# Kernel optimization log

Measured on AMD Instinct MI355X. Metric: run time of the kernel, lower is better.

The kernel has to match this reference:

```python
import jax, jax.numpy as jnp
import numpy as np

B, X, C = 8192, 8, 512        # batch, map_num, img_dim==tex_dim
P, Y = 8, 1000                # n_prompts, cls_num
FAKE = 16                     # fake prompt width (hardcoded in module)
F = 2048                      # feat_dim
CLS = 1000                    # cls_num
IN_DIM = P * X * FAKE         # 1024
SF = 64.0


def setup_inputs() -> dict:
    key = jax.random.key(0)
    ks = jax.random.split(key, 8)
    s = 0.02
    return {
        "img_f": jax.random.normal(ks[0], (B, X, C), jnp.float32),
        "tex_f": jax.random.normal(ks[1], (P, Y, C), jnp.float32),
        "fake_cls": jax.random.normal(ks[2], (P, FAKE, C), jnp.float32),
        "fc_w": jax.random.normal(ks[3], (C, C), jnp.float32) * s,
        "fc_b": jnp.zeros((C,), jnp.float32),
        "bn1_g": jnp.ones((IN_DIM,), jnp.float32),
        "bn1_b": jnp.zeros((IN_DIM,), jnp.float32),
        "w1": jax.random.normal(ks[4], (F, IN_DIM), jnp.float32) * s,
        "b1": jnp.zeros((F,), jnp.float32),
        "bn2_g": jnp.ones((F,), jnp.float32),
        "bn2_b": jnp.zeros((F,), jnp.float32),
        "w2": jax.random.normal(ks[5], (CLS, F), jnp.float32) * s,
        "b2": jnp.zeros((CLS,), jnp.float32),
    }


def _bn(x, g, b, eps=1e-5):
    # BatchNorm1d in training mode: batch mean / biased batch var
    m = x.mean(axis=0)
    v = x.var(axis=0)
    return (x - m) * jax.lax.rsqrt(v + eps) * g + b


def reference(img_f, tex_f, fake_cls, fc_w, fc_b, bn1_g, bn1_b, w1, b1,
              bn2_g, bn2_b, w2, b2):
    # independent L2 norm over feature dim, scaled by x_sf=64
    img_n = img_f / (jnp.linalg.norm(img_f, axis=-1, keepdims=True) + 1e-6) * SF
    tex_n = tex_f / (jnp.linalg.norm(tex_f, axis=-1, keepdims=True) + 1e-6) * SF
    # prompt attention over the class axis
    tex_fc = jnp.einsum('pyc,dc->pyd', tex_n, fc_w) + fc_b          # fc(tex_f)
    attn = jax.nn.softmax(jnp.einsum('pxc,pyc->pxy', fake_cls, tex_fc), axis=-1)
    tex_a = jnp.einsum('pxy,pyc->pxc', attn, tex_n)                  # (P,16,C)
    # cross-modal relation: 'b x c, y d c -> b yxd' (icomp/tcomp are Identity)
    cp = jnp.einsum('bxc,pdc->bpxd', img_n, tex_a).reshape(img_n.shape[0], -1)
    # prt_fc: BN -> Linear -> ELU -> BN -> Linear
    h = jax.nn.elu(_bn(cp, bn1_g, bn1_b) @ w1.T + b1)
    return _bn(h, bn2_g, bn2_b) @ w2.T + b2
```

## Files before the change

kernel.cpp:

```cpp
#include <hip/hip_runtime.h>
#include <math.h>


typedef __attribute__((ext_vector_type(8))) short bf16x8;
typedef __attribute__((ext_vector_type(4))) float f32x4;

__device__ __forceinline__ float waveSum(float v) {
#pragma unroll
    for (int o = 32; o > 0; o >>= 1) v += __shfl_xor(v, o);
    return v;
}
__device__ __forceinline__ float waveMax(float v) {
#pragma unroll
    for (int o = 32; o > 0; o >>= 1) v = fmaxf(v, __shfl_xor(v, o));
    return v;
}
__device__ __forceinline__ unsigned short f2bf(float x) {
    union { float f; unsigned u; } v; v.f = x;
    unsigned r = v.u + 0x7FFFu + ((v.u >> 16) & 1u);
    return (unsigned short)(r >> 16);
}
__device__ __forceinline__ float bf2f(unsigned short h) {
    union { unsigned u; float f; } v; v.u = ((unsigned)h) << 16; return v.f;
}
__device__ __forceinline__ void gload16(const void* g, const void* l) {
    __builtin_amdgcn_global_load_lds((const __attribute__((address_space(1))) void*)g,
                                     (__attribute__((address_space(3))) void*)l, 16, 0, 0);
}
__device__ __forceinline__ int xcd_swz(int d, int n) {
    int q = n >> 3;
    return (d & 7) * q + (d >> 3);
}
#define SBAR __builtin_amdgcn_sched_barrier(0)

__global__ __launch_bounds__(256) void k_prep(const float* __restrict__ tex_f,
                                              unsigned short* __restrict__ texn,
                                              const float* __restrict__ fake_cls,
                                              const float* __restrict__ fc_w,
                                              unsigned short* __restrict__ g_bf) {
    __shared__ float sred[4];
    __shared__ float fcls[512];
    int bid = blockIdx.x, t = threadIdx.x;
    if (bid < 8000) {
        const float* r = tex_f + (size_t)bid * 512;
        float2 v = *(const float2*)(r + t * 2);
        float ss = v.x * v.x + v.y * v.y;
        ss = waveSum(ss);
        if ((t & 63) == 0) sred[t >> 6] = ss;
        __syncthreads();
        float tot = sred[0] + sred[1] + sred[2] + sred[3];
        float sc = 64.f / (sqrtf(tot) + 1e-6f);
        unsigned u = (unsigned)f2bf(v.x * sc) | ((unsigned)f2bf(v.y * sc) << 16);
        *(unsigned*)(texn + (size_t)bid * 512 + t * 2) = u;
    } else {
        int row = bid - 8000;
        fcls[t]       = fake_cls[row * 512 + t];
        fcls[t + 256] = fake_cls[row * 512 + t + 256];
        __syncthreads();
        float a0 = 0.f, a1 = 0.f;
        for (int d = 0; d < 512; ++d) {
            float fv = fcls[d];
            a0 = fmaf(fv, fc_w[d * 512 + t], a0);
            a1 = fmaf(fv, fc_w[d * 512 + t + 256], a1);
        }
        g_bf[row * 512 + t]       = f2bf(a0);
        g_bf[row * 512 + t + 256] = f2bf(a1);
    }
}

__global__ __launch_bounds__(256) void k_wsum_sm(const float* __restrict__ logit,
                                                 const unsigned short* __restrict__ texn,
                                                 float* __restrict__ part) {
    int yt = blockIdx.x, p = blockIdx.y, t = threadIdx.x;
    int lane = t & 63, w = t >> 6;
    __shared__ float wl[16][63];
    __shared__ float ms[16], iss[16];
    const int y0 = yt * 63;
    const int ylen = min(63, 1000 - y0);
#pragma unroll
    for (int rr = 0; rr < 4; ++rr) {
        int x = w * 4 + rr;
        const float* lr = logit + ((size_t)p * 16 + x) * 1000;
        float m = -3.0e38f;
        for (int y = lane; y < 1000; y += 64) m = fmaxf(m, lr[y]);
        m = waveMax(m);
        float s = 0.f;
        for (int y = lane; y < 1000; y += 64) s += expf(lr[y] - m);
        s = waveSum(s);
        if (lane == 0) { ms[x] = m; iss[x] = 1.f / s; }
    }
    __syncthreads();
    for (int idx = t; idx < 16 * ylen; idx += 256) {
        int x = idx / ylen, y = idx % ylen;
        wl[x][y] = expf(logit[((size_t)p * 16 + x) * 1000 + y0 + y] - ms[x]) * iss[x];
    }
    __syncthreads();
    int c0 = t * 2;
    const unsigned short* tp = texn + ((size_t)p * 1000 + y0) * 512 + c0;
    float a0[16], a1[16];
#pragma unroll
    for (int x = 0; x < 16; ++x) { a0[x] = 0.f; a1[x] = 0.f; }
    for (int y = 0; y < ylen; ++y) {
        unsigned u = *(const unsigned*)(tp + (size_t)y * 512);
        float lo = bf2f((unsigned short)(u & 0xffff));
        float hi = bf2f((unsigned short)(u >> 16));
#pragma unroll
        for (int x = 0; x < 16; ++x) {
            float ww = wl[x][y];
            a0[x] = fmaf(ww, lo, a0[x]);
            a1[x] = fmaf(ww, hi, a1[x]);
        }
    }
#pragma unroll
    for (int x = 0; x < 16; ++x) {
        float* dst = part + ((size_t)((yt * 8 + p) * 16 + x)) * 512 + c0;
        dst[0] = a0[x];
        dst[1] = a1[x];
    }
}

__global__ __launch_bounds__(256) void k_texa_red(const float* __restrict__ part,
                                                  unsigned short* __restrict__ texa) {
    int row = blockIdx.x, t = threadIdx.x;
    int p = row >> 4, x = row & 15;
    int c = t * 2;
    float s0 = 0.f, s1 = 0.f;
#pragma unroll
    for (int yt = 0; yt < 16; ++yt) {
        const float* src = part + ((size_t)((yt * 8 + p) * 16 + x)) * 512 + c;
        s0 += src[0];
        s1 += src[1];
    }
    unsigned u = (unsigned)f2bf(s0) | ((unsigned)f2bf(s1) << 16);
    *(unsigned*)(texa + (size_t)row * 512 + c) = u;
}

__global__ __launch_bounds__(256) void k_colstat_bf(const unsigned short* __restrict__ src,
                                                    float* __restrict__ ps,
                                                    float* __restrict__ pq, int ncols) {
    int col = blockIdx.x * 256 + threadIdx.x;
    int r0 = blockIdx.y * 128;
    const unsigned short* p = src + (size_t)r0 * ncols + col;
    float s = 0.f, q = 0.f;
    for (int r = 0; r < 128; ++r) {
        float v = bf2f(p[(size_t)r * ncols]);
        s += v;
        q = fmaf(v, v, q);
    }
    ps[(size_t)blockIdx.y * ncols + col] = s;
    pq[(size_t)blockIdx.y * ncols + col] = q;
}

template <bool PERM>
__global__ __launch_bounds__(256) void k_bnfin(const float* __restrict__ ps,
                                               const float* __restrict__ pq,
                                               const float* __restrict__ gam,
                                               const float* __restrict__ bet,
                                               float* __restrict__ a, float* __restrict__ c,
                                               int ncols) {
    int col = blockIdx.x * 256 + threadIdx.x;
    float S = 0.f, Q = 0.f;
    for (int i = 0; i < 64; ++i) {
        S += ps[(size_t)i * ncols + col];
        Q += pq[(size_t)i * ncols + col];
    }
    float mean = S * (1.f / 8192.f);
    float var = Q * (1.f / 8192.f) - mean * mean;
    int j = col;
    if (PERM) {
        int x = col >> 7, jj = col & 127, pp = jj >> 4, d = jj & 15;
        j = (pp << 7) + (x << 4) + d;
    }
    float av = gam[j] * rsqrtf(var + 1e-5f);
    a[col] = av;
    c[col] = bet[j] - mean * av;
}

template <bool PERM>
__global__ __launch_bounds__(256) void k_foldw_bf(const float* __restrict__ W,
                                                  const float* __restrict__ bin,
                                                  const float* __restrict__ a,
                                                  const float* __restrict__ c,
                                                  unsigned short* __restrict__ Wout,
                                                  float* __restrict__ bout,
                                                  int Kdim, int nvalid) {
    int f = blockIdx.x, t = threadIdx.x;
    unsigned short* wo = Wout + (size_t)f * Kdim;
    if (f >= nvalid) {
        for (int col = t; col < Kdim; col += 256) wo[col] = 0;
        if (t == 0) bout[f] = 0.f;
        return;
    }
    const float* wr = W + (size_t)f * Kdim;
    float partial = 0.f;
    for (int col = t; col < Kdim; col += 256) {
        int j = col;
        if (PERM) {
            int x = col >> 7, jj = col & 127, pp = jj >> 4, d = jj & 15;
            j = (pp << 7) + (x << 4) + d;
        }
        float wv = wr[j];
        wo[col] = f2bf(wv * a[col]);
        partial = fmaf(wv, c[col], partial);
    }
    partial = waveSum(partial);
    __shared__ float sred[4];
    if ((t & 63) == 0) sred[t >> 6] = partial;
    __syncthreads();
    if (t == 0) bout[f] = bin[f] + sred[0] + sred[1] + sred[2] + sred[3];
}

template <int EPI, bool A_F32>
__global__ __launch_bounds__(256) void gemm_mfma(const void* __restrict__ Av,
                                                 const unsigned short* __restrict__ Bv,
                                                 void* __restrict__ Cv, int K,
                                                 int ntn, int ldc, int nvalid,
                                                 int aZ, int bZ, int cZ) {
    __shared__ unsigned short Asl[128 * 64];
    __shared__ unsigned short Bsl[128 * 64];
    __shared__ float rowinv[128];
    const int tid = threadIdx.x;
    const int lane = tid & 63, wid = tid >> 6;
    const int wr = wid >> 1, wc = wid & 1;
    const int wg = xcd_swz(blockIdx.x, gridDim.x);
    const int m0 = (wg / ntn) * 128, n0 = (wg % ntn) * 128;
    const int z = blockIdx.y;

    const float* Af = (const float*)Av;
    const unsigned short* Ab = (const unsigned short*)Av + (size_t)z * aZ;
    const unsigned short* B = Bv + (size_t)z * bZ;

    f32x4 acc[4][4];
#pragma unroll
    for (int i = 0; i < 4; ++i)
#pragma unroll
        for (int j = 0; j < 4; ++j) acc[i][j] = {0.f, 0.f, 0.f, 0.f};

    const int swz = ((lane & 7) ^ (lane >> 3)) * 8;
    const int lrow = lane & 15, lkh = lane >> 4;
    float ssq[4] = {0.f, 0.f, 0.f, 0.f};

    for (int k0 = 0; k0 < K; k0 += 64) {
        if (A_F32) {
#pragma unroll
            for (int r = 0; r < 4; ++r) {
                int row = r * 32 + (tid >> 3);
                int kk = (tid & 7) * 8;
                const float* src = Af + (size_t)(m0 + row) * K + k0 + kk;
                float4 p0 = *(const float4*)src;
                float4 p1 = *(const float4*)(src + 4);
                ssq[r] += p0.x*p0.x + p0.y*p0.y + p0.z*p0.z + p0.w*p0.w
                        + p1.x*p1.x + p1.y*p1.y + p1.z*p1.z + p1.w*p1.w;
                bf16x8 v;
                v[0] = (short)f2bf(p0.x); v[1] = (short)f2bf(p0.y);
                v[2] = (short)f2bf(p0.z); v[3] = (short)f2bf(p0.w);
                v[4] = (short)f2bf(p1.x); v[5] = (short)f2bf(p1.y);
                v[6] = (short)f2bf(p1.z); v[7] = (short)f2bf(p1.w);
                *(bf16x8*)&Asl[row * 64 + (kk ^ ((row & 7) << 3))] = v;
            }
        } else {
#pragma unroll
            for (int r = 0; r < 4; ++r) {
                int row = r * 32 + wid * 8 + (lane >> 3);
                gload16(Ab + (size_t)(m0 + row) * K + k0 + swz,
                        Asl + r * 2048 + wid * 512);
            }
        }
#pragma unroll
        for (int r = 0; r < 4; ++r) {
            int row = r * 32 + wid * 8 + (lane >> 3);
            gload16(B + (size_t)(n0 + row) * K + k0 + swz,
                    Bsl + r * 2048 + wid * 512);
        }
        __syncthreads();
#pragma unroll
        for (int kk = 0; kk < 2; ++kk) {
            bf16x8 af[4], bfr[4];
#pragma unroll
            for (int m = 0; m < 4; ++m) {
                int row = wr * 64 + m * 16 + lrow;
                af[m] = *(const bf16x8*)&Asl[row * 64 + ((kk * 32 + lkh * 8) ^ ((row & 7) << 3))];
            }
#pragma unroll
            for (int n = 0; n < 4; ++n) {
                int row = wc * 64 + n * 16 + lrow;
                bfr[n] = *(const bf16x8*)&Bsl[row * 64 + ((kk * 32 + lkh * 8) ^ ((row & 7) << 3))];
            }
#pragma unroll
            for (int m = 0; m < 4; ++m)
#pragma unroll
                for (int n = 0; n < 4; ++n)
                    acc[m][n] = __builtin_amdgcn_mfma_f32_16x16x32_bf16(af[m], bfr[n], acc[m][n], 0, 0, 0);
        }
        __syncthreads();
    }

    if (A_F32) {
#pragma unroll
        for (int r = 0; r < 4; ++r) {
            float s = ssq[r];
            s += __shfl_xor(s, 1); s += __shfl_xor(s, 2); s += __shfl_xor(s, 4);
            if ((tid & 7) == 0) rowinv[r * 32 + (tid >> 3)] = 64.f / (sqrtf(s) + 1e-6f);
        }
        __syncthreads();
    }

    const int colbase = n0 + wc * 64 + lrow;
    if (EPI == 0) {
        unsigned short* C = (unsigned short*)Cv;
#pragma unroll
        for (int m = 0; m < 4; ++m) {
            int rloc = wr * 64 + m * 16 + lkh * 4;
#pragma unroll
            for (int r = 0; r < 4; ++r) {
                float riv = rowinv[rloc + r];
#pragma unroll
                for (int n = 0; n < 4; ++n)
                    C[(size_t)(m0 + rloc + r) * ldc + colbase + n * 16] = f2bf(acc[m][n][r] * riv);
            }
        }
    } else {
        float* C = (float*)Cv + (size_t)z * cZ;
#pragma unroll
        for (int m = 0; m < 4; ++m) {
            int row = m0 + wr * 64 + m * 16 + lkh * 4;
#pragma unroll
            for (int r = 0; r < 4; ++r) {
                if ((row + r) >= 16) continue;
#pragma unroll
                for (int n = 0; n < 4; ++n) {
                    int col = colbase + n * 16;
                    if (col < nvalid) C[(size_t)(row + r) * ldc + col] = acc[m][n][r];
                }
            }
        }
    }
}

template <int FM, int NH, int EPI>
__global__ __launch_bounds__(512, 2) void gemm256(const unsigned short* __restrict__ A,
                                                  const unsigned short* __restrict__ B,
                                                  void* __restrict__ Cv, int K,
                                                  int ntn, int ldc, int nvalid,
                                                  const float* __restrict__ bias,
                                                  float* __restrict__ ps,
                                                  float* __restrict__ pq) {
    constexpr int BM = FM * 32;
    constexpr int MH = BM / 128;
    constexpr int BN = NH * 128;
    constexpr int LA = 2 * (MH + NH);
    __shared__ unsigned short Asl[2][MH][128 * 64];
    __shared__ unsigned short Bsl[2][NH][128 * 64];
    const int tid = threadIdx.x;
    const int lane = tid & 63, wid = tid >> 6;
    const int wm = wid >> 2, wn = wid & 3;
    const int wg = xcd_swz(blockIdx.x, gridDim.x);
    const int m0 = (wg / ntn) * BM, n0 = (wg % ntn) * BN;
    const int lrow = lane & 15, lkh = lane >> 4;
    const int l7 = lane & 7;
    const int ksrc = ((lane & 7) ^ (lane >> 3)) * 8;
    const int mbase = wm * (BM / 2);
    const int mhalf = mbase >> 7;
    const int mloc0 = mbase & 127;
    const int nbase = wn * 64;
    const int nhalf = nbase >> 7;
    const int nloc0 = nbase & 127;

    f32x4 acc[FM][4];
#pragma unroll
    for (int m = 0; m < FM; ++m)
#pragma unroll
        for (int n = 0; n < 4; ++n) acc[m][n] = {0.f, 0.f, 0.f, 0.f};

    const int nkt = K >> 6;

    auto stage = [&](int kt, int buf) {
#pragma unroll
        for (int hf = 0; hf < MH; ++hf)
#pragma unroll
            for (int j = 0; j < 2; ++j) {
                int rl = wid * 16 + j * 8 + (lane >> 3);
                gload16(A + (size_t)(m0 + hf * 128 + rl) * K + kt * 64 + ksrc,
                        &Asl[buf][hf][(wid * 16 + j * 8) * 64]);
            }
#pragma unroll
        for (int hf = 0; hf < NH; ++hf)
#pragma unroll
            for (int j = 0; j < 2; ++j) {
                int rl = wid * 16 + j * 8 + (lane >> 3);
                gload16(B + (size_t)(n0 + hf * 128 + rl) * K + kt * 64 + ksrc,
                        &Bsl[buf][hf][(wid * 16 + j * 8) * 64]);
            }
    };

    stage(0, 0);
    stage(1, 1);
    if constexpr (LA == 8) asm volatile("s_waitcnt vmcnt(8)" ::: "memory");
    else asm volatile("s_waitcnt vmcnt(6)" ::: "memory");
    SBAR; __builtin_amdgcn_s_barrier(); SBAR;

    for (int kt = 0; kt < nkt; ++kt) {
        const int cur = kt & 1;
        bf16x8 af0[FM], bf0[4];
#pragma unroll
        for (int m = 0; m < FM; ++m) {
            int row = mloc0 + m * 16 + lrow;
            af0[m] = *(const bf16x8*)&Asl[cur][mhalf][row * 64 + ((lkh ^ l7) << 3)];
        }
#pragma unroll
        for (int n = 0; n < 4; ++n) {
            int row = nloc0 + n * 16 + lrow;
            bf0[n] = *(const bf16x8*)&Bsl[cur][nhalf][row * 64 + ((lkh ^ l7) << 3)];
        }
        __builtin_amdgcn_s_setprio(1);
#pragma unroll
        for (int m = 0; m < FM; ++m)
#pragma unroll
            for (int n = 0; n < 4; ++n)
                acc[m][n] = __builtin_amdgcn_mfma_f32_16x16x32_bf16(af0[m], bf0[n], acc[m][n], 0, 0, 0);
        __builtin_amdgcn_s_setprio(0);
        bf16x8 af1[FM], bf1[4];
#pragma unroll
        for (int m = 0; m < FM; ++m) {
            int row = mloc0 + m * 16 + lrow;
            af1[m] = *(const bf16x8*)&Asl[cur][mhalf][row * 64 + (((4 + lkh) ^ l7) << 3)];
        }
#pragma unroll
        for (int n = 0; n < 4; ++n) {
            int row = nloc0 + n * 16 + lrow;
            bf1[n] = *(const bf16x8*)&Bsl[cur][nhalf][row * 64 + (((4 + lkh) ^ l7) << 3)];
        }
        if (kt + 1 < nkt) {
            asm volatile("s_waitcnt lgkmcnt(0)" ::: "memory");
            SBAR; __builtin_amdgcn_s_barrier(); SBAR;
            if (kt + 2 < nkt) {
                stage(kt + 2, cur);
                if constexpr (LA == 8) asm volatile("s_waitcnt vmcnt(8)" ::: "memory");
                else asm volatile("s_waitcnt vmcnt(6)" ::: "memory");
            } else {
                asm volatile("s_waitcnt vmcnt(0)" ::: "memory");
            }
            SBAR; __builtin_amdgcn_s_barrier(); SBAR;
        }
        __builtin_amdgcn_s_setprio(1);
#pragma unroll
        for (int m = 0; m < FM; ++m)
#pragma unroll
            for (int n = 0; n < 4; ++n)
                acc[m][n] = __builtin_amdgcn_mfma_f32_16x16x32_bf16(af1[m], bf1[n], acc[m][n], 0, 0, 0);
        __builtin_amdgcn_s_setprio(0);
    }

    const int colbase = n0 + nbase + lrow;
    if (EPI == 1) {
        unsigned short* C = (unsigned short*)Cv;
        float bv[4], sN[4] = {0.f, 0.f, 0.f, 0.f}, qN[4] = {0.f, 0.f, 0.f, 0.f};
#pragma unroll
        for (int n = 0; n < 4; ++n) bv[n] = bias[colbase + n * 16];
#pragma unroll
        for (int m = 0; m < FM; ++m) {
            int row = m0 + mbase + m * 16 + lkh * 4;
#pragma unroll
            for (int r = 0; r < 4; ++r)
#pragma unroll
                for (int n = 0; n < 4; ++n) {
                    float v = acc[m][n][r] + bv[n];
                    v = v > 0.f ? v : expm1f(v);
                    sN[n] += v;
                    qN[n] = fmaf(v, v, qN[n]);
                    C[(size_t)(row + r) * ldc + colbase + n * 16] = f2bf(v);
                }
        }
#pragma unroll
        for (int n = 0; n < 4; ++n) {
            sN[n] += __shfl_xor(sN[n], 16); sN[n] += __shfl_xor(sN[n], 32);
            qN[n] += __shfl_xor(qN[n], 16); qN[n] += __shfl_xor(qN[n], 32);
        }
        if (lane < 16) {
            int mt = wg / ntn;
#pragma unroll
            for (int n = 0; n < 4; ++n) {
                ps[(size_t)(mt * 2 + wm) * ldc + colbase + n * 16] = sN[n];
                pq[(size_t)(mt * 2 + wm) * ldc + colbase + n * 16] = qN[n];
            }
        }
    } else {
        float* C = (float*)Cv;
        float bv[4];
#pragma unroll
        for (int n = 0; n < 4; ++n) bv[n] = bias[colbase + n * 16];
#pragma unroll
        for (int m = 0; m < FM; ++m) {
            int row = m0 + mbase + m * 16 + lkh * 4;
#pragma unroll
            for (int r = 0; r < 4; ++r)
#pragma unroll
                for (int n = 0; n < 4; ++n) {
                    int col = colbase + n * 16;
                    if (col < nvalid) C[(size_t)(row + r) * ldc + col] = acc[m][n][r] + bv[n];
                }
        }
    }
}

extern "C" void kernel_launch(void* const* d_in, const int* in_sizes, int n_in,
                              void* d_out, int out_size, void* d_ws, size_t ws_size,
                              hipStream_t stream) {
    const float* img_f    = (const float*)d_in[0];
    const float* tex_f    = (const float*)d_in[1];
    const float* fake_cls = (const float*)d_in[2];
    const float* fc_w     = (const float*)d_in[3];
    const float* bn1_g    = (const float*)d_in[5];
    const float* bn1_b    = (const float*)d_in[6];
    const float* w1       = (const float*)d_in[7];
    const float* b1       = (const float*)d_in[8];
    const float* bn2_g    = (const float*)d_in[9];
    const float* bn2_b    = (const float*)d_in[10];
    const float* w2       = (const float*)d_in[11];
    const float* b2       = (const float*)d_in[12];
    float* out = (float*)d_out;

    char* w = (char*)d_ws;
    unsigned short* texn = (unsigned short*)(w);
    unsigned short* g_bf = (unsigned short*)(w + 8388608);
    float*          logit= (float*)(w + 8650752);
    float*          part = (float*)(w + 9175040);
    unsigned short* texa = (unsigned short*)(w + 13369344);
    unsigned short* cp   = (unsigned short*)(w + 13500416);
    unsigned short* w1a  = (unsigned short*)(w + 30277632);
    float*          b1p  = (float*)(w + 34471936);
    float*          a1   = (float*)(w + 34480128);
    float*          c1   = (float*)(w + 34484224);
    float*          ps   = (float*)(w + 34488320);
    float*          pq   = (float*)(w + 35012608);
    unsigned short* h    = (unsigned short*)(w + 35536896);
    unsigned short* w2a  = (unsigned short*)(w + 69091328);
    float*          b2p  = (float*)(w + 73285632);
    float*          a2   = (float*)(w + 73289728);
    float*          c2   = (float*)(w + 73297920);

    k_prep<<<8128, 256, 0, stream>>>(tex_f, texn, fake_cls, fc_w, g_bf);
    gemm_mfma<3, false><<<dim3(8, 8), 256, 0, stream>>>(
        g_bf, texn, logit, 512, 8, 1000, 1000, 16 * 512, 1000 * 512, 16 * 1000);
    k_wsum_sm<<<dim3(16, 8), 256, 0, stream>>>(logit, texn, part);
    k_texa_red<<<128, 256, 0, stream>>>(part, texa);

    gemm_mfma<0, true><<<dim3(512, 1), 256, 0, stream>>>(
        img_f, texa, cp, 512, 1, 128, 128, 0, 0, 0);

    k_colstat_bf<<<dim3(4, 64), 256, 0, stream>>>(cp, ps, pq, 1024);
    k_bnfin<true><<<4, 256, 0, stream>>>(ps, pq, bn1_g, bn1_b, a1, c1, 1024);
    k_foldw_bf<true><<<2048, 256, 0, stream>>>(w1, b1, a1, c1, w1a, b1p, 1024, 2048);

    gemm256<8, 2, 1><<<dim3(256), 512, 0, stream>>>(
        cp, w1a, h, 1024, 8, 2048, 2048, b1p, ps, pq);

    k_bnfin<false><<<8, 256, 0, stream>>>(ps, pq, bn2_g, bn2_b, a2, c2, 2048);
    k_foldw_bf<false><<<1024, 256, 0, stream>>>(w2, b2, a2, c2, w2a, b2p, 2048, 1000);

    gemm256<4, 2, 2><<<dim3(256), 512, 0, stream>>>(
        h, w2a, out, 2048, 4, 1000, 1000, b2p, nullptr, nullptr);
}
```

Before: 240.8 us.

## Interleave next-tile global loads with second-half MFMAs in gemm256 loop

Splits the tile staging into separate A and B load lambdas and issues them between two halves of the second-k-slice MFMA block, before the vmcnt wait and barrier. Previously all loads were issued and waited on before any of those MFMAs ran. The goal is to hide global-to-LDS load issue latency behind matrix math and shorten the sync bubble. It also hardcodes BN as 256, which assumes NH==2 for every instantiation, and it moves the MFMAs after the first barrier, which changes where the waves stall.

```diff
diff --git a/kernel.cpp b/kernel.cpp
--- a/kernel.cpp
+++ b/kernel.cpp
@@ -347,7 +347,6 @@
                                                   float* __restrict__ pq) {
     constexpr int BM = FM * 32;
     constexpr int MH = BM / 128;
-    constexpr int BN = NH * 128;
     constexpr int LA = 2 * (MH + NH);
     __shared__ unsigned short Asl[2][MH][128 * 64];
     __shared__ unsigned short Bsl[2][NH][128 * 64];
@@ -355,7 +354,7 @@
     const int lane = tid & 63, wid = tid >> 6;
     const int wm = wid >> 2, wn = wid & 3;
     const int wg = xcd_swz(blockIdx.x, gridDim.x);
-    const int m0 = (wg / ntn) * BM, n0 = (wg % ntn) * BN;
+    const int m0 = (wg / ntn) * BM, n0 = (wg % ntn) * 256;
     const int lrow = lane & 15, lkh = lane >> 4;
     const int l7 = lane & 7;
     const int ksrc = ((lane & 7) ^ (lane >> 3)) * 8;
@@ -374,7 +373,7 @@
 
     const int nkt = K >> 6;
 
-    auto stage = [&](int kt, int buf) {
+    auto stageA = [&](int kt, int buf) {
 #pragma unroll
         for (int hf = 0; hf < MH; ++hf)
 #pragma unroll
@@ -383,6 +382,8 @@
                 gload16(A + (size_t)(m0 + hf * 128 + rl) * K + kt * 64 + ksrc,
                         &Asl[buf][hf][(wid * 16 + j * 8) * 64]);
             }
+    };
+    auto stageB = [&](int kt, int buf) {
 #pragma unroll
         for (int hf = 0; hf < NH; ++hf)
 #pragma unroll
@@ -393,10 +394,9 @@
             }
     };
 
-    stage(0, 0);
-    stage(1, 1);
-    if constexpr (LA == 8) asm volatile("s_waitcnt vmcnt(8)" ::: "memory");
-    else asm volatile("s_waitcnt vmcnt(6)" ::: "memory");
+    stageA(0, 0); stageB(0, 0);
+    stageA(1, 1); stageB(1, 1);
+    asm volatile("s_waitcnt vmcnt(%0)" :: "i"(LA) : "memory");
     SBAR; __builtin_amdgcn_s_barrier(); SBAR;
 
     for (int kt = 0; kt < nkt; ++kt) {
@@ -433,22 +433,37 @@
         if (kt + 1 < nkt) {
             asm volatile("s_waitcnt lgkmcnt(0)" ::: "memory");
             SBAR; __builtin_amdgcn_s_barrier(); SBAR;
-            if (kt + 2 < nkt) {
-                stage(kt + 2, cur);
-                if constexpr (LA == 8) asm volatile("s_waitcnt vmcnt(8)" ::: "memory");
-                else asm volatile("s_waitcnt vmcnt(6)" ::: "memory");
-            } else {
-                asm volatile("s_waitcnt vmcnt(0)" ::: "memory");
-            }
+            const bool pf = (kt + 2 < nkt);
+            if (pf) stageA(kt + 2, cur);
+            SBAR;
+            __builtin_amdgcn_s_setprio(1);
+#pragma unroll
+            for (int m = 0; m < FM / 2; ++m)
+#pragma unroll
+                for (int n = 0; n < 4; ++n)
+                    acc[m][n] = __builtin_amdgcn_mfma_f32_16x16x32_bf16(af1[m], bf1[n], acc[m][n], 0, 0, 0);
+            __builtin_amdgcn_s_setprio(0);
+            if (pf) stageB(kt + 2, cur);
+            SBAR;
+            __builtin_amdgcn_s_setprio(1);
+#pragma unroll
+            for (int m = FM / 2; m < FM; ++m)
+#pragma unroll
+                for (int n = 0; n < 4; ++n)
+                    acc[m][n] = __builtin_amdgcn_mfma_f32_16x16x32_bf16(af1[m], bf1[n], acc[m][n], 0, 0, 0);
+            __builtin_amdgcn_s_setprio(0);
+            if (pf) asm volatile("s_waitcnt vmcnt(%0)" :: "i"(LA) : "memory");
+            else    asm volatile("s_waitcnt vmcnt(0)" ::: "memory");
             SBAR; __builtin_amdgcn_s_barrier(); SBAR;
-        }
-        __builtin_amdgcn_s_setprio(1);
-#pragma unroll
-        for (int m = 0; m < FM; ++m)
-#pragma unroll
-            for (int n = 0; n < 4; ++n)
-                acc[m][n] = __builtin_amdgcn_mfma_f32_16x16x32_bf16(af1[m], bf1[n], acc[m][n], 0, 0, 0);
-        __builtin_amdgcn_s_setprio(0);
+        } else {
+            __builtin_amdgcn_s_setprio(1);
+#pragma unroll
+            for (int m = 0; m < FM; ++m)
+#pragma unroll
+                for (int n = 0; n < 4; ++n)
+                    acc[m][n] = __builtin_amdgcn_mfma_f32_16x16x32_bf16(af1[m], bf1[n], acc[m][n], 0, 0, 0);
+            __builtin_amdgcn_s_setprio(0);
+        }
     }
 
     const int colbase = n0 + nbase + lrow;
```

New measurement: 488.0 us. +102.6%, slower.
